# Kernel tuning notes

Measured on AMD Instinct MI355X. Metric: run time of the kernel, lower is better.

## Reference

```python
import jax, jax.numpy as jnp
import numpy as np

N, E = 500000, 128
H1, H2, H3, OUT = 256, 128, 64, 1
IN = 3 * E


def setup_inputs() -> dict:
    key = jax.random.key(0)
    ks = jax.random.split(key, 12)
    s = 0.02
    return {
        "encoder": jax.random.normal(ks[0], (N, E), dtype=jnp.float32),
        "current_state_tsr": jax.random.randint(ks[1], (N, 1), 0, 2, dtype=jnp.int32),
        "W1": jax.random.normal(ks[2], (IN, H1), dtype=jnp.float32) * s,
        "b1": jnp.zeros((H1,), dtype=jnp.float32),
        "W2": jax.random.normal(ks[3], (H1, H2), dtype=jnp.float32) * s,
        "b2": jnp.zeros((H2,), dtype=jnp.float32),
        "W3": jax.random.normal(ks[4], (H2, H3), dtype=jnp.float32) * s,
        "b3": jnp.zeros((H3,), dtype=jnp.float32),
        "W4": jax.random.normal(ks[5], (H3, OUT), dtype=jnp.float32) * s,
        "b4": jnp.zeros((OUT,), dtype=jnp.float32),
        "graph": 1,
    }


def reference(encoder, current_state_tsr, W1, b1, W2, b2, W3, b3, W4, b4, graph):
    n = encoder.shape[0]
    cs = current_state_tsr  # [N,1] int state flags
    # masked node features (zeros where mask fails), then single-graph max readout
    in_state = jnp.where(cs > 0, encoder, 0.0)            # [N,E]
    mu_in = jax.nn.relu(jnp.max(in_state, axis=0, keepdims=True))   # [1,E]
    not_in_state = jnp.where(cs == 0, encoder, 0.0)       # [N,E]
    mu_not = jax.nn.relu(jnp.max(not_in_state, axis=0, keepdims=True))  # [1,E]
    feats = jnp.concatenate(
        [jnp.broadcast_to(mu_in, (n, mu_in.shape[1])),
         jnp.broadcast_to(mu_not, (n, mu_not.shape[1])),
         encoder], axis=1)                                # [N,3E]
    h = jax.nn.leaky_relu(feats @ W1 + b1)
    h = jax.nn.leaky_relu(h @ W2 + b2)
    h = jax.nn.leaky_relu(h @ W3 + b3)
    logits = h @ W4 + b4                                  # [N,1]
    q = jax.nn.softmax(logits, axis=0)                    # softmax across nodes
    return q.squeeze(axis=1)                              # [N]
```

## Files before the change

### kernel.cpp

```cpp
#include <hip/hip_runtime.h>
#include <hip/hip_bf16.h>

#define NN 500000
#define NBLK_CM 2000

typedef unsigned short ushort_t;
typedef __attribute__((ext_vector_type(8))) __bf16 bf16x8;
typedef __attribute__((ext_vector_type(2))) __bf16 bf16x2;
typedef __attribute__((ext_vector_type(4))) float f32x4;
typedef __attribute__((ext_vector_type(4))) unsigned uint4v;

__device__ inline ushort_t f2bf(float f) {
  unsigned u = __builtin_bit_cast(unsigned, f);
  return (ushort_t)((u + 0x7FFFu + ((u >> 16) & 1u)) >> 16);
}
__device__ inline float lrelu(float v) { return fmaxf(v, 0.f) + 0.01f * fminf(v, 0.f); }
__device__ inline unsigned pk2(float lo, float hi) {
  bf16x2 v; v[0] = (__bf16)lo; v[1] = (__bf16)hi;
  return __builtin_bit_cast(unsigned, v);
}
__device__ inline bf16x8 mk8(unsigned w0, unsigned w1, unsigned w2, unsigned w3) {
  uint4v u; u.x = w0; u.y = w1; u.z = w2; u.w = w3;
  return __builtin_bit_cast(bf16x8, u);
}
#define SHF_X(v, m) ((unsigned)__shfl_xor((int)(v), (m), 64))
#define SBAR() __builtin_amdgcn_sched_barrier(0)

__device__ inline void bfly4(unsigned q0, unsigned q1, unsigned q2, unsigned q3,
                             bool b0, bool b1,
                             unsigned& w0, unsigned& w1, unsigned& w2, unsigned& w3)
{
  unsigned vA0 = b1 ? q0 : q2, vA1 = b1 ? q1 : q3;
  unsigned eA0 = SHF_X(vA0, 32), eA1 = SHF_X(vA1, 32);
  unsigned s00 = b1 ? eA0 : q0, s01 = b1 ? eA1 : q1;
  unsigned s10 = b1 ? q2 : eA0, s11 = b1 ? q3 : eA1;
  unsigned vB0 = b0 ? s00 : s10, vB1 = b0 ? s01 : s11;
  unsigned eB0 = SHF_X(vB0, 16), eB1 = SHF_X(vB1, 16);
  w0 = b0 ? eB0 : s00; w1 = b0 ? eB1 : s01;
  w2 = b0 ? s10 : eB0; w3 = b0 ? s11 : eB1;
}

__global__ __launch_bounds__(256) void k_colmax(
    const float* __restrict__ enc, const int* __restrict__ cs,
    float* __restrict__ partials)
{
  __shared__ float4 s_in[256], s_not[256];
  const int tid = threadIdx.x;
  const int c4 = tid & 31;
  const int rs = tid >> 5;
  const long base = (long)blockIdx.x * 250;
  float4 mi = {0.f, 0.f, 0.f, 0.f}, mn = {0.f, 0.f, 0.f, 0.f};
  const float4* e4 = (const float4*)enc;
  #pragma unroll 4
  for (int it = 0; it < 32; ++it) {
    long r = base + rs + 8L * it;
    if (r < base + 250 && r < NN) {
      float4 v = e4[r * 32 + c4];
      bool ins = cs[r] > 0;
      mi.x = fmaxf(mi.x, ins ? v.x : 0.f); mi.y = fmaxf(mi.y, ins ? v.y : 0.f);
      mi.z = fmaxf(mi.z, ins ? v.z : 0.f); mi.w = fmaxf(mi.w, ins ? v.w : 0.f);
      mn.x = fmaxf(mn.x, ins ? 0.f : v.x); mn.y = fmaxf(mn.y, ins ? 0.f : v.y);
      mn.z = fmaxf(mn.z, ins ? 0.f : v.z); mn.w = fmaxf(mn.w, ins ? 0.f : v.w);
    }
  }
  s_in[tid] = mi; s_not[tid] = mn;
  __syncthreads();
  if (tid < 32) {
    for (int j = 1; j < 8; ++j) {
      float4 a = s_in[j * 32 + tid], b = s_not[j * 32 + tid];
      mi.x = fmaxf(mi.x, a.x); mi.y = fmaxf(mi.y, a.y);
      mi.z = fmaxf(mi.z, a.z); mi.w = fmaxf(mi.w, a.w);
      mn.x = fmaxf(mn.x, b.x); mn.y = fmaxf(mn.y, b.y);
      mn.z = fmaxf(mn.z, b.z); mn.w = fmaxf(mn.w, b.w);
    }
    float* po = partials + (size_t)blockIdx.x * 256;
    ((float4*)po)[tid] = mi;
    ((float4*)(po + 128))[tid] = mn;
  }
}

__global__ __launch_bounds__(256) void k_red1(
    const float* __restrict__ partials, float* __restrict__ red2)
{
  const int tid = threadIdx.x, b = blockIdx.x;
  float m = 0.f;
  #pragma unroll 8
  for (int row = b; row < NBLK_CM; row += 64)
    m = fmaxf(m, partials[(size_t)row * 256 + tid]);
  red2[b * 256 + tid] = m;
}

__global__ __launch_bounds__(1024) void k_red2(
    const float* __restrict__ red2,
    float* __restrict__ mu_in, float* __restrict__ mu_not)
{
  __shared__ float sT[1024];
  const int tid = threadIdx.x;
  const int col = tid & 255, sl = tid >> 8;
  float m = 0.f;
  #pragma unroll
  for (int j = 0; j < 16; ++j)
    m = fmaxf(m, red2[(sl * 16 + j) * 256 + col]);
  sT[tid] = m;
  __syncthreads();
  if (tid < 256) {
    m = fmaxf(fmaxf(sT[tid], sT[tid + 256]), fmaxf(sT[tid + 512], sT[tid + 768]));
    if (tid < 128) mu_in[tid] = m;
    else           mu_not[tid - 128] = m;
  }
}

__global__ __launch_bounds__(512)
__attribute__((amdgpu_waves_per_eu(2, 2)))
void k_mlp(
    const float* __restrict__ enc,
    const float* __restrict__ W1, const float* __restrict__ b1,
    const float* __restrict__ W2, const float* __restrict__ b2,
    const float* __restrict__ W3, const float* __restrict__ b3,
    const float* __restrict__ W4, const float* __restrict__ b4,
    const float* __restrict__ mu_in, const float* __restrict__ mu_not,
    float* __restrict__ eL, float* __restrict__ psum)
{
  __shared__ ushort_t sW1[256 * 128];
  __shared__ ushort_t sW2[128 * 256];
  __shared__ ushort_t sW3[64 * 128];
  __shared__ float sC[520];
  __shared__ float sT[512];

  const int tid = threadIdx.x;

  for (int idx = tid; idx < 32768; idx += 512) {
    int n = idx & 255, k = idx >> 8;
    int bp = ((k >> 3) + 2 * n) & 15;
    sW1[n * 128 + bp * 8 + (k & 7)] = f2bf(W1[(256 + k) * 256 + n]);
  }
  for (int idx = tid; idx < 32768; idx += 512) {
    int n = idx & 127, k = idx >> 7;
    int bp = ((k >> 3) + 2 * n) & 31;
    sW2[n * 256 + bp * 8 + (k & 7)] = f2bf(W2[k * 128 + n]);
  }
  for (int idx = tid; idx < 8192; idx += 512) {
    int n = idx & 63, k = idx >> 6;
    int bp = ((k >> 3) + 2 * n) & 15;
    sW3[n * 128 + bp * 8 + (k & 7)] = f2bf(W3[k * 64 + n]);
  }
  if (tid >= 256 && tid < 384) sC[tid] = b2[tid - 256];
  else if (tid >= 384 && tid < 448) sC[tid] = b3[tid - 384];
  else if (tid >= 448) sC[tid] = W4[tid - 448];
  if (tid == 0) sC[512] = b4[0];
  {
    const int j = tid & 255, h = tid >> 8;
    float c = h ? 0.f : b1[j];
    #pragma unroll 8
    for (int e = 64 * h; e < 64 * h + 64; ++e) {
      c += mu_in[e]  * W1[e * 256 + j];
      c += mu_not[e] * W1[(128 + e) * 256 + j];
    }
    sT[tid] = c;
  }
  __syncthreads();
  if (tid < 256) sC[tid] = sT[tid] + sT[tid + 256];
  __syncthreads();

  const int wave = tid >> 6, lane = tid & 63;
  const int lr = lane & 15, lg = lane >> 4;
  const int wid = blockIdx.x * 8 + wave;
  const bool b0 = lg & 1, b1f = lg & 2;
  const int sw = lg + 2 * lr;

  const ushort_t* w1p = sW1 + lr * 128;
  const ushort_t* w2p = sW2 + lr * 256;
  const ushort_t* w3p = sW3 + lr * 128;

  float es = 0.f;
  bf16x8 B1a[4], B1b[4];

  {
    const float4* pa = (const float4*)(enc + (size_t)(wid * 32 + lr) * 128);
    const float4* pb = (const float4*)(enc + (size_t)(wid * 32 + 16 + lr) * 128);
    #pragma unroll
    for (int kt = 0; kt < 4; ++kt) {
      float4 f0 = pa[kt * 8 + lg * 2], f1 = pa[kt * 8 + lg * 2 + 1];
      float4 g0 = pb[kt * 8 + lg * 2], g1 = pb[kt * 8 + lg * 2 + 1];
      bf16x8 a, b;
      a[0] = (__bf16)f0.x; a[1] = (__bf16)f0.y; a[2] = (__bf16)f0.z; a[3] = (__bf16)f0.w;
      a[4] = (__bf16)f1.x; a[5] = (__bf16)f1.y; a[6] = (__bf16)f1.z; a[7] = (__bf16)f1.w;
      b[0] = (__bf16)g0.x; b[1] = (__bf16)g0.y; b[2] = (__bf16)g0.z; b[3] = (__bf16)g0.w;
      b[4] = (__bf16)g1.x; b[5] = (__bf16)g1.y; b[6] = (__bf16)g1.z; b[7] = (__bf16)g1.w;
      B1a[kt] = a; B1b[kt] = b;
    }
  }

  for (int r0 = wid * 32; r0 < NN; r0 += 65536) {
    bf16x8 B2a[8], B2b[8];
    #pragma unroll
    for (int p = 0; p < 8; ++p) {
      f32x4 aA0 = (f32x4){0.f,0.f,0.f,0.f}, aA1 = (f32x4){0.f,0.f,0.f,0.f};
      f32x4 aB0 = (f32x4){0.f,0.f,0.f,0.f}, aB1 = (f32x4){0.f,0.f,0.f,0.f};
      #pragma unroll
      for (int kt = 0; kt < 4; ++kt) {
        bf16x8 wA = *(const bf16x8*)(w1p + (2 * p) * 2048 + (((4 * kt + sw) & 15) << 3));
        bf16x8 wB = *(const bf16x8*)(w1p + (2 * p + 1) * 2048 + (((4 * kt + sw) & 15) << 3));
        aA0 = __builtin_amdgcn_mfma_f32_16x16x32_bf16(wA, B1a[kt], aA0, 0, 0, 0);
        aA1 = __builtin_amdgcn_mfma_f32_16x16x32_bf16(wB, B1a[kt], aA1, 0, 0, 0);
        aB0 = __builtin_amdgcn_mfma_f32_16x16x32_bf16(wA, B1b[kt], aB0, 0, 0, 0);
        aB1 = __builtin_amdgcn_mfma_f32_16x16x32_bf16(wB, B1b[kt], aB1, 0, 0, 0);
      }
      float4 cb0 = *(const float4*)(sC + 16 * (2 * p) + 4 * lg);
      float4 cb1 = *(const float4*)(sC + 16 * (2 * p + 1) + 4 * lg);
      {
        unsigned q0 = pk2(lrelu(aA0[0] + cb0.x), lrelu(aA0[1] + cb0.y));
        unsigned q1 = pk2(lrelu(aA0[2] + cb0.z), lrelu(aA0[3] + cb0.w));
        unsigned q2 = pk2(lrelu(aA1[0] + cb1.x), lrelu(aA1[1] + cb1.y));
        unsigned q3 = pk2(lrelu(aA1[2] + cb1.z), lrelu(aA1[3] + cb1.w));
        unsigned w0, w1, w2, w3;
        bfly4(q0, q1, q2, q3, b0, b1f, w0, w1, w2, w3);
        B2a[p] = mk8(w0, w1, w2, w3);
      }
      {
        unsigned q0 = pk2(lrelu(aB0[0] + cb0.x), lrelu(aB0[1] + cb0.y));
        unsigned q1 = pk2(lrelu(aB0[2] + cb0.z), lrelu(aB0[3] + cb0.w));
        unsigned q2 = pk2(lrelu(aB1[0] + cb1.x), lrelu(aB1[1] + cb1.y));
        unsigned q3 = pk2(lrelu(aB1[2] + cb1.z), lrelu(aB1[3] + cb1.w));
        unsigned w0, w1, w2, w3;
        bfly4(q0, q1, q2, q3, b0, b1f, w0, w1, w2, w3);
        B2b[p] = mk8(w0, w1, w2, w3);
      }
    }
    SBAR();
    bf16x8 B3a[4], B3b[4];
    #pragma unroll
    for (int p = 0; p < 4; ++p) {
      f32x4 aA0 = (f32x4){0.f,0.f,0.f,0.f}, aA1 = (f32x4){0.f,0.f,0.f,0.f};
      f32x4 aB0 = (f32x4){0.f,0.f,0.f,0.f}, aB1 = (f32x4){0.f,0.f,0.f,0.f};
      #pragma unroll
      for (int kt = 0; kt < 8; ++kt) {
        bf16x8 wA = *(const bf16x8*)(w2p + (2 * p) * 4096 + (((4 * kt + sw) & 31) << 3));
        bf16x8 wB = *(const bf16x8*)(w2p + (2 * p + 1) * 4096 + (((4 * kt + sw) & 31) << 3));
        aA0 = __builtin_amdgcn_mfma_f32_16x16x32_bf16(wA, B2a[kt], aA0, 0, 0, 0);
        aA1 = __builtin_amdgcn_mfma_f32_16x16x32_bf16(wB, B2a[kt], aA1, 0, 0, 0);
        aB0 = __builtin_amdgcn_mfma_f32_16x16x32_bf16(wA, B2b[kt], aB0, 0, 0, 0);
        aB1 = __builtin_amdgcn_mfma_f32_16x16x32_bf16(wB, B2b[kt], aB1, 0, 0, 0);
      }
      float4 cb0 = *(const float4*)(sC + 256 + 16 * (2 * p) + 4 * lg);
      float4 cb1 = *(const float4*)(sC + 256 + 16 * (2 * p + 1) + 4 * lg);
      {
        unsigned q0 = pk2(lrelu(aA0[0] + cb0.x), lrelu(aA0[1] + cb0.y));
        unsigned q1 = pk2(lrelu(aA0[2] + cb0.z), lrelu(aA0[3] + cb0.w));
        unsigned q2 = pk2(lrelu(aA1[0] + cb1.x), lrelu(aA1[1] + cb1.y));
        unsigned q3 = pk2(lrelu(aA1[2] + cb1.z), lrelu(aA1[3] + cb1.w));
        unsigned w0, w1, w2, w3;
        bfly4(q0, q1, q2, q3, b0, b1f, w0, w1, w2, w3);
        B3a[p] = mk8(w0, w1, w2, w3);
      }
      {
        unsigned q0 = pk2(lrelu(aB0[0] + cb0.x), lrelu(aB0[1] + cb0.y));
        unsigned q1 = pk2(lrelu(aB0[2] + cb0.z), lrelu(aB0[3] + cb0.w));
        unsigned q2 = pk2(lrelu(aB1[0] + cb1.x), lrelu(aB1[1] + cb1.y));
        unsigned q3 = pk2(lrelu(aB1[2] + cb1.z), lrelu(aB1[3] + cb1.w));
        unsigned w0, w1, w2, w3;
        bfly4(q0, q1, q2, q3, b0, b1f, w0, w1, w2, w3);
        B3b[p] = mk8(w0, w1, w2, w3);
      }
    }
    SBAR();
    int rn = r0 + 65536; if (rn >= NN) rn = r0;
    float4 tA[8], tB[8];
    {
      const float4* pa = (const float4*)(enc + (size_t)(rn + lr) * 128);
      const float4* pb = (const float4*)(enc + (size_t)(rn + 16 + lr) * 128);
      #pragma unroll
      for (int kt = 0; kt < 4; ++kt) {
        tA[2 * kt]     = pa[kt * 8 + lg * 2];
        tA[2 * kt + 1] = pa[kt * 8 + lg * 2 + 1];
        tB[2 * kt]     = pb[kt * 8 + lg * 2];
        tB[2 * kt + 1] = pb[kt * 8 + lg * 2 + 1];
      }
    }
    SBAR();
    float da = 0.f, db = 0.f;
    #pragma unroll
    for (int p = 0; p < 2; ++p) {
      f32x4 aA0 = (f32x4){0.f,0.f,0.f,0.f}, aA1 = (f32x4){0.f,0.f,0.f,0.f};
      f32x4 aB0 = (f32x4){0.f,0.f,0.f,0.f}, aB1 = (f32x4){0.f,0.f,0.f,0.f};
      #pragma unroll
      for (int kt = 0; kt < 4; ++kt) {
        bf16x8 wA = *(const bf16x8*)(w3p + (2 * p) * 2048 + (((4 * kt + sw) & 15) << 3));
        bf16x8 wB = *(const bf16x8*)(w3p + (2 * p + 1) * 2048 + (((4 * kt + sw) & 15) << 3));
        aA0 = __builtin_amdgcn_mfma_f32_16x16x32_bf16(wA, B3a[kt], aA0, 0, 0, 0);
        aA1 = __builtin_amdgcn_mfma_f32_16x16x32_bf16(wB, B3a[kt], aA1, 0, 0, 0);
        aB0 = __builtin_amdgcn_mfma_f32_16x16x32_bf16(wA, B3b[kt], aB0, 0, 0, 0);
        aB1 = __builtin_amdgcn_mfma_f32_16x16x32_bf16(wB, B3b[kt], aB1, 0, 0, 0);
      }
      float4 cb0  = *(const float4*)(sC + 384 + 16 * (2 * p) + 4 * lg);
      float4 cb1  = *(const float4*)(sC + 384 + 16 * (2 * p + 1) + 4 * lg);
      float4 w4v0 = *(const float4*)(sC + 448 + 16 * (2 * p) + 4 * lg);
      float4 w4v1 = *(const float4*)(sC + 448 + 16 * (2 * p + 1) + 4 * lg);
      da += lrelu(aA0[0] + cb0.x) * w4v0.x + lrelu(aA0[1] + cb0.y) * w4v0.y
          + lrelu(aA0[2] + cb0.z) * w4v0.z + lrelu(aA0[3] + cb0.w) * w4v0.w;
      da += lrelu(aA1[0] + cb1.x) * w4v1.x + lrelu(aA1[1] + cb1.y) * w4v1.y
          + lrelu(aA1[2] + cb1.z) * w4v1.z + lrelu(aA1[3] + cb1.w) * w4v1.w;
      db += lrelu(aB0[0] + cb0.x) * w4v0.x + lrelu(aB0[1] + cb0.y) * w4v0.y
          + lrelu(aB0[2] + cb0.z) * w4v0.z + lrelu(aB0[3] + cb0.w) * w4v0.w;
      db += lrelu(aB1[0] + cb1.x) * w4v1.x + lrelu(aB1[1] + cb1.y) * w4v1.y
          + lrelu(aB1[2] + cb1.z) * w4v1.z + lrelu(aB1[3] + cb1.w) * w4v1.w;
    }
    da += __shfl_xor(da, 16, 64); da += __shfl_xor(da, 32, 64);
    db += __shfl_xor(db, 16, 64); db += __shfl_xor(db, 32, 64);
    float eva = expf(da + sC[512]), evb = expf(db + sC[512]);
    if (lg == 0) { eL[r0 + lr] = eva; eL[r0 + 16 + lr] = evb; }
    es += eva + evb;
    #pragma unroll
    for (int kt = 0; kt < 4; ++kt) {
      float4 f0 = tA[2 * kt], f1 = tA[2 * kt + 1];
      float4 g0 = tB[2 * kt], g1 = tB[2 * kt + 1];
      bf16x8 a, b;
      a[0] = (__bf16)f0.x; a[1] = (__bf16)f0.y; a[2] = (__bf16)f0.z; a[3] = (__bf16)f0.w;
      a[4] = (__bf16)f1.x; a[5] = (__bf16)f1.y; a[6] = (__bf16)f1.z; a[7] = (__bf16)f1.w;
      b[0] = (__bf16)g0.x; b[1] = (__bf16)g0.y; b[2] = (__bf16)g0.z; b[3] = (__bf16)g0.w;
      b[4] = (__bf16)g1.x; b[5] = (__bf16)g1.y; b[6] = (__bf16)g1.z; b[7] = (__bf16)g1.w;
      B1a[kt] = a; B1b[kt] = b;
    }
  }
  #pragma unroll
  for (int off = 1; off < 64; off <<= 1) es += __shfl_xor(es, off, 64);
  if (lane == 0) psum[wid] = 0.25f * es;
}

__global__ __launch_bounds__(256) void k_finalsum(const float* __restrict__ psum,
                                                  float* __restrict__ scal)
{
  const int tid = threadIdx.x;
  float s = 0.f;
  #pragma unroll
  for (int k = 0; k < 8; ++k) s += psum[tid + k * 256];
  #pragma unroll
  for (int off = 1; off < 64; off <<= 1) s += __shfl_xor(s, off, 64);
  __shared__ float sr[4];
  if ((tid & 63) == 0) sr[tid >> 6] = s;
  __syncthreads();
  if (tid == 0) scal[0] = 1.f / (sr[0] + sr[1] + sr[2] + sr[3]);
}

__global__ __launch_bounds__(256) void k_norm(const float* __restrict__ eL,
                                              const float* __restrict__ scal,
                                              float* __restrict__ out)
{
  const float inv = scal[0];
  const int i = blockIdx.x * 256 + threadIdx.x;
  if (i < NN / 4) {
    float4 v = ((const float4*)eL)[i];
    float4 o = {v.x * inv, v.y * inv, v.z * inv, v.w * inv};
    ((float4*)out)[i] = o;
  }
}

extern "C" void kernel_launch(void* const* d_in, const int* in_sizes, int n_in,
                              void* d_out, int out_size, void* d_ws, size_t ws_size,
                              hipStream_t stream) {
  const float* enc = (const float*)d_in[0];
  const int*   cs  = (const int*)d_in[1];
  const float* W1  = (const float*)d_in[2];
  const float* b1  = (const float*)d_in[3];
  const float* W2  = (const float*)d_in[4];
  const float* b2  = (const float*)d_in[5];
  const float* W3  = (const float*)d_in[6];
  const float* b3  = (const float*)d_in[7];
  const float* W4  = (const float*)d_in[8];
  const float* b4  = (const float*)d_in[9];
  float* out = (float*)d_out;

  char* ws = (char*)d_ws;
  float* mu_in  = (float*)(ws + 0);
  float* mu_not = (float*)(ws + 512);
  float* psum   = (float*)(ws + 2048);
  float* scal   = (float*)(ws + 10240);
  float* red2   = (float*)(ws + 16384);
  float* eLbuf  = (float*)(ws + 131072);
  float* partials = (float*)(ws + 131072);

  k_colmax<<<dim3(NBLK_CM), dim3(256), 0, stream>>>(enc, cs, partials);
  k_red1<<<dim3(64), dim3(256), 0, stream>>>(partials, red2);
  k_red2<<<dim3(1), dim3(1024), 0, stream>>>(red2, mu_in, mu_not);
  k_mlp<<<dim3(256), dim3(512), 0, stream>>>(enc, W1, b1, W2, b2, W3, b3, W4, b4,
                                             mu_in, mu_not, eLbuf, psum);
  k_finalsum<<<dim3(1), dim3(256), 0, stream>>>(psum, scal);
  k_norm<<<dim3(489), dim3(256), 0, stream>>>(eLbuf, scal, out);
}
```

Baseline: 171.8 us.

## Fuse final sum into norm kernel, reverse row loop, add MFMA priority hints

```diff
diff --git a/kernel.cpp b/kernel.cpp
--- a/kernel.cpp
+++ b/kernel.cpp
@@ -25,6 +25,7 @@
 }
 #define SHF_X(v, m) ((unsigned)__shfl_xor((int)(v), (m), 64))
 #define SBAR() __builtin_amdgcn_sched_barrier(0)
+#define PRIO(n) __builtin_amdgcn_s_setprio(n)
 
 __device__ inline void bfly4(unsigned q0, unsigned q1, unsigned q2, unsigned q3,
                              bool b0, bool b1,
@@ -175,9 +176,12 @@
   float es = 0.f;
   bf16x8 B1a[4], B1b[4];
 
+  const int it_hi = (NN - 1 - wid * 32) / 65536;
+
   {
-    const float4* pa = (const float4*)(enc + (size_t)(wid * 32 + lr) * 128);
-    const float4* pb = (const float4*)(enc + (size_t)(wid * 32 + 16 + lr) * 128);
+    const int r0 = wid * 32 + it_hi * 65536;
+    const float4* pa = (const float4*)(enc + (size_t)(r0 + lr) * 128);
+    const float4* pb = (const float4*)(enc + (size_t)(r0 + 16 + lr) * 128);
     #pragma unroll
     for (int kt = 0; kt < 4; ++kt) {
       float4 f0 = pa[kt * 8 + lg * 2], f1 = pa[kt * 8 + lg * 2 + 1];
@@ -191,12 +195,14 @@
     }
   }
 
-  for (int r0 = wid * 32; r0 < NN; r0 += 65536) {
+  for (int it = it_hi; it >= 0; --it) {
+    const int r0 = wid * 32 + it * 65536;
     bf16x8 B2a[8], B2b[8];
     #pragma unroll
     for (int p = 0; p < 8; ++p) {
       f32x4 aA0 = (f32x4){0.f,0.f,0.f,0.f}, aA1 = (f32x4){0.f,0.f,0.f,0.f};
       f32x4 aB0 = (f32x4){0.f,0.f,0.f,0.f}, aB1 = (f32x4){0.f,0.f,0.f,0.f};
+      PRIO(1);
       #pragma unroll
       for (int kt = 0; kt < 4; ++kt) {
         bf16x8 wA = *(const bf16x8*)(w1p + (2 * p) * 2048 + (((4 * kt + sw) & 15) << 3));
@@ -206,6 +212,7 @@
         aB0 = __builtin_amdgcn_mfma_f32_16x16x32_bf16(wA, B1b[kt], aB0, 0, 0, 0);
         aB1 = __builtin_amdgcn_mfma_f32_16x16x32_bf16(wB, B1b[kt], aB1, 0, 0, 0);
       }
+      PRIO(0);
       float4 cb0 = *(const float4*)(sC + 16 * (2 * p) + 4 * lg);
       float4 cb1 = *(const float4*)(sC + 16 * (2 * p + 1) + 4 * lg);
       {
@@ -233,6 +240,7 @@
     for (int p = 0; p < 4; ++p) {
       f32x4 aA0 = (f32x4){0.f,0.f,0.f,0.f}, aA1 = (f32x4){0.f,0.f,0.f,0.f};
       f32x4 aB0 = (f32x4){0.f,0.f,0.f,0.f}, aB1 = (f32x4){0.f,0.f,0.f,0.f};
+      PRIO(1);
       #pragma unroll
       for (int kt = 0; kt < 8; ++kt) {
         bf16x8 wA = *(const bf16x8*)(w2p + (2 * p) * 4096 + (((4 * kt + sw) & 31) << 3));
@@ -242,6 +250,7 @@
         aB0 = __builtin_amdgcn_mfma_f32_16x16x32_bf16(wA, B2b[kt], aB0, 0, 0, 0);
         aB1 = __builtin_amdgcn_mfma_f32_16x16x32_bf16(wB, B2b[kt], aB1, 0, 0, 0);
       }
+      PRIO(0);
       float4 cb0 = *(const float4*)(sC + 256 + 16 * (2 * p) + 4 * lg);
       float4 cb1 = *(const float4*)(sC + 256 + 16 * (2 * p + 1) + 4 * lg);
       {
@@ -264,7 +273,7 @@
       }
     }
     SBAR();
-    int rn = r0 + 65536; if (rn >= NN) rn = r0;
+    const int rn = (it > 0) ? (r0 - 65536) : r0;
     float4 tA[8], tB[8];
     {
       const float4* pa = (const float4*)(enc + (size_t)(rn + lr) * 128);
@@ -283,6 +292,7 @@
     for (int p = 0; p < 2; ++p) {
       f32x4 aA0 = (f32x4){0.f,0.f,0.f,0.f}, aA1 = (f32x4){0.f,0.f,0.f,0.f};
       f32x4 aB0 = (f32x4){0.f,0.f,0.f,0.f}, aB1 = (f32x4){0.f,0.f,0.f,0.f};
+      PRIO(1);
       #pragma unroll
       for (int kt = 0; kt < 4; ++kt) {
         bf16x8 wA = *(const bf16x8*)(w3p + (2 * p) * 2048 + (((4 * kt + sw) & 15) << 3));
@@ -292,6 +302,7 @@
         aB0 = __builtin_amdgcn_mfma_f32_16x16x32_bf16(wA, B3b[kt], aB0, 0, 0, 0);
         aB1 = __builtin_amdgcn_mfma_f32_16x16x32_bf16(wB, B3b[kt], aB1, 0, 0, 0);
       }
+      PRIO(0);
       float4 cb0  = *(const float4*)(sC + 384 + 16 * (2 * p) + 4 * lg);
       float4 cb1  = *(const float4*)(sC + 384 + 16 * (2 * p + 1) + 4 * lg);
       float4 w4v0 = *(const float4*)(sC + 448 + 16 * (2 * p) + 4 * lg);
@@ -327,27 +338,21 @@
   if (lane == 0) psum[wid] = 0.25f * es;
 }
 
-__global__ __launch_bounds__(256) void k_finalsum(const float* __restrict__ psum,
-                                                  float* __restrict__ scal)
-{
+__global__ __launch_bounds__(256) void k_norm(const float* __restrict__ eL,
+                                              const float* __restrict__ psum,
+                                              float* __restrict__ out)
+{
+  __shared__ float sr[4];
   const int tid = threadIdx.x;
   float s = 0.f;
   #pragma unroll
   for (int k = 0; k < 8; ++k) s += psum[tid + k * 256];
   #pragma unroll
   for (int off = 1; off < 64; off <<= 1) s += __shfl_xor(s, off, 64);
-  __shared__ float sr[4];
   if ((tid & 63) == 0) sr[tid >> 6] = s;
   __syncthreads();
-  if (tid == 0) scal[0] = 1.f / (sr[0] + sr[1] + sr[2] + sr[3]);
-}
-
-__global__ __launch_bounds__(256) void k_norm(const float* __restrict__ eL,
-                                              const float* __restrict__ scal,
-                                              float* __restrict__ out)
-{
-  const float inv = scal[0];
-  const int i = blockIdx.x * 256 + threadIdx.x;
+  const float inv = 1.f / (sr[0] + sr[1] + sr[2] + sr[3]);
+  const int i = blockIdx.x * 256 + tid;
   if (i < NN / 4) {
     float4 v = ((const float4*)eL)[i];
     float4 o = {v.x * inv, v.y * inv, v.z * inv, v.w * inv};
@@ -374,7 +379,6 @@
   float* mu_in  = (float*)(ws + 0);
   float* mu_not = (float*)(ws + 512);
   float* psum   = (float*)(ws + 2048);
-  float* scal   = (float*)(ws + 10240);
   float* red2   = (float*)(ws + 16384);
   float* eLbuf  = (float*)(ws + 131072);
   float* partials = (float*)(ws + 131072);
@@ -384,6 +388,5 @@
   k_red2<<<dim3(1), dim3(1024), 0, stream>>>(red2, mu_in, mu_not);
   k_mlp<<<dim3(256), dim3(512), 0, stream>>>(enc, W1, b1, W2, b2, W3, b3, W4, b4,
                                              mu_in, mu_not, eLbuf, psum);
-  k_finalsum<<<dim3(1), dim3(256), 0, stream>>>(psum, scal);
-  k_norm<<<dim3(489), dim3(256), 0, stream>>>(eLbuf, scal, out);
-}
+  k_norm<<<dim3(489), dim3(256), 0, stream>>>(eLbuf, psum, out);
+}
```

After: 171.0 us. About the same (-0.5%).
